# Kernel optimization log

Measured on AMD Instinct MI355X. Metric: run time of the kernel, lower is better.

## Reference

```python
import jax, jax.numpy as jnp
import numpy as np
from jax import lax

DIM = 64           # LHMSA dim
C3 = 3 * DIM       # high-band channels
HEADS = C3 // 32   # 6
WS = 8             # window size
SHIFT = 4          # shift size
EPS = 1e-6


def _ln_chw(x, w, b):
    # channel-last layer norm applied to BCHW input over C
    xt = x.transpose(0, 2, 3, 1)
    mu = xt.mean(-1, keepdims=True)
    var = ((xt - mu) ** 2).mean(-1, keepdims=True)
    y = (xt - mu) / jnp.sqrt(var + EPS) * w + b
    return y.transpose(0, 3, 1, 2)


def _conv1x1(x, w):
    # w: (out_c, in_c), no bias
    return jnp.einsum('bchw,oc->bohw', x, w)


def _dwconv3(x, w):
    # depthwise 3x3, w: (C,1,3,3)
    C = x.shape[1]
    return lax.conv_general_dilated(x, w, (1, 1), ((1, 1), (1, 1)),
                                    dimension_numbers=('NCHW', 'OIHW', 'NCHW'),
                                    feature_group_count=C)


def _gelu(x):
    return jax.nn.gelu(x, approximate=False)


def _dwt(x):
    x01 = x[:, :, 0::2, :] * 0.5
    x02 = x[:, :, 1::2, :] * 0.5
    x1 = x01[:, :, :, 0::2]; x2 = x02[:, :, :, 0::2]
    x3 = x01[:, :, :, 1::2]; x4 = x02[:, :, :, 1::2]
    ll = x1 + x2 + x3 + x4
    high = jnp.concatenate([-x1 - x2 + x3 + x4,
                            -x1 + x2 - x3 + x4,
                            x1 - x2 - x3 + x4], axis=1)
    return ll, high


def _iwt(ll, high):
    B, C, H, W = ll.shape
    hl, lh, hh = jnp.split(high, 3, axis=1)
    x1 = (ll - hl - lh + hh) * 0.5
    x2 = (ll - hl + lh - hh) * 0.5
    x3 = (ll + hl - lh - hh) * 0.5
    x4 = (ll + hl + lh + hh) * 0.5
    even = jnp.stack([x1, x3], axis=-1).reshape(B, C, H, 2 * W)  # rows 0::2
    odd = jnp.stack([x2, x4], axis=-1).reshape(B, C, H, 2 * W)   # rows 1::2
    return jnp.stack([even, odd], axis=-2).reshape(B, C, 2 * H, 2 * W)


def _swin_mhsa(x, qkv_w, qkv_b, proj_w, proj_b, rpb_table, rpi):
    # x: (B, C3, H, W); H,W divisible by WS -> no padding path
    B, C, H, W = x.shape
    dh = C // HEADS
    scale = dh ** (-0.5)
    xh = x.transpose(0, 2, 3, 1)                           # BHWC
    xh = jnp.roll(xh, (-SHIFT, -SHIFT), axis=(1, 2))
    nh, nw = H // WS, W // WS
    xw = xh.reshape(B, nh, WS, nw, WS, C).transpose(0, 1, 3, 2, 4, 5)
    xw = xw.reshape(B * nh * nw, WS * WS, C)               # (nW, N, C)
    qkv = xw @ qkv_w.T + qkv_b                             # (nW, N, 3C)
    qkv = qkv.reshape(-1, WS * WS, 3, HEADS, dh).transpose(2, 0, 3, 1, 4)
    q, k, v = qkv[0], qkv[1], qkv[2]                       # (nW, h, N, dh)
    attn = jnp.einsum('whnd,whmd->whnm', q, k) * scale
    bias = rpb_table[rpi.reshape(-1)].reshape(WS * WS, WS * WS, HEADS)
    attn = jax.nn.softmax(attn + bias.transpose(2, 0, 1)[None], axis=-1)
    out = jnp.einsum('whnm,whmd->whnd', attn, v)
    out = out.transpose(0, 2, 1, 3).reshape(-1, WS * WS, C)
    out = out.reshape(B, nh, nw, WS, WS, C).transpose(0, 1, 3, 2, 4, 5)
    out = out.reshape(B, H, W, C)
    out = jnp.roll(out, (SHIFT, SHIFT), axis=(1, 2))
    out = out @ proj_w.T + proj_b
    return out.transpose(0, 3, 1, 2)


def _rel_pos_index():
    coords = np.stack(np.meshgrid(np.arange(WS), np.arange(WS), indexing='ij'))
    cf = coords.reshape(2, -1)
    rel = (cf[:, :, None] - cf[:, None, :]).transpose(1, 2, 0).astype(np.int64)
    rel[:, :, 0] += WS - 1
    rel[:, :, 1] += WS - 1
    rel[:, :, 0] *= 2 * WS - 1
    return rel.sum(-1)


def setup_inputs() -> dict:
    key = jax.random.key(0)
    ks = jax.random.split(key, 12)
    B, H, W = 2, 512, 512
    x = jax.random.normal(ks[0], (B, DIM, H, W), jnp.float32)
    s = 0.02
    inp = {
        'x': x,
        'norm_w': jnp.ones((C3,), jnp.float32),
        'norm_b': jnp.zeros((C3,), jnp.float32),
        'qkv_w': jax.random.normal(ks[1], (3 * C3, C3), jnp.float32) * s,
        'qkv_b': jnp.zeros((3 * C3,), jnp.float32),
        'proj_w': jax.random.normal(ks[2], (C3, C3), jnp.float32) * s,
        'proj_b': jnp.zeros((C3,), jnp.float32),
        'rpb_table': jax.random.normal(ks[3], ((2 * WS - 1) ** 2, HEADS), jnp.float32) * s,
        'aux_dw_w': jax.random.normal(ks[4], (DIM, 1, 3, 3), jnp.float32) * 0.1,
        'aux_pw_w': jax.random.normal(ks[5], (DIM, DIM), jnp.float32) * s,
        'cg1_w': jax.random.normal(ks[6], (C3 * 3 // 12, DIM), jnp.float32) * s,
        'cg2_w': jax.random.normal(ks[7], (C3, C3 * 3 // 12), jnp.float32) * s,
        'po_w': jax.random.normal(ks[8], (DIM, DIM), jnp.float32) * s,
        'gamma_main': jnp.full((1,), 1e-4, jnp.float32),
        'gamma_aux': jnp.full((1,), 0.5, jnp.float32),
        'gamma_cross': jnp.full((1,), 1e-5, jnp.float32),
        'rel_pos_index': jnp.asarray(_rel_pos_index(), jnp.int32),
    }
    return inp


def reference(x, norm_w, norm_b, qkv_w, qkv_b, proj_w, proj_b, rpb_table,
              aux_dw_w, aux_pw_w, cg1_w, cg2_w, po_w,
              gamma_main, gamma_aux, gamma_cross, rel_pos_index):
    ll, high = _dwt(x)
    high_norm = _ln_chw(high, norm_w, norm_b)
    refined_high = high + gamma_main * _swin_mhsa(high_norm, qkv_w, qkv_b,
                                                  proj_w, proj_b, rpb_table,
                                                  rel_pos_index)
    refined_ll = ll + gamma_aux * _conv1x1(_gelu(_dwconv3(ll, aux_dw_w)), aux_pw_w)
    gap = ll.mean((2, 3), keepdims=True)
    cross = jax.nn.sigmoid(_conv1x1(_gelu(_conv1x1(gap, cg1_w)), cg2_w))
    refined_high = refined_high * (1.0 + gamma_cross * (cross - 0.5) * 2.0)
    out = _iwt(refined_ll, refined_high)
    return _conv1x1(out - x, po_w)
```

## Files before the change

### kernel.cpp

```cpp
#include <hip/hip_runtime.h>
#include <hip/hip_bf16.h>
#include <math.h>

typedef __hip_bfloat16 bf16;
typedef short s8v __attribute__((ext_vector_type(8)));
typedef float f4v __attribute__((ext_vector_type(4)));
#define MFMA16(a,b,c) __builtin_amdgcn_mfma_f32_16x16x32_bf16(a,b,c,0,0,0)

#define B2   2
#define C64  64
#define C3   192
#define HEADS 6
#define NWIN 2048

#define P_NORMW 0
#define P_NORMB 192
#define P_QKVW  384
#define P_QKVB  110976
#define P_PROJW 111552
#define P_PROJB 148416
#define P_RPB   148608
#define P_AUXDW 149958
#define P_AUXPW 150534
#define P_CG1   154630
#define P_CG2   157702
#define P_PO    166918
#define P_GM    171014
#define P_GA    171015
#define P_GC    171016

#define WS_FLAG   0
#define WS_PARAMS 256
#define WS_GAP    684544
#define WS_AMUL   685568
#define WS_CVAL   687616
#define WS_TSTAT  689664
#define WS_LL     1738240
#define WS_DLLW   18515456
#define WS_WOUT   35292672
#define WS_HRAW   85624320
#define WS_WQKV   135955968
#define WS_WPROJ  136177152
#define WS_WPW    136250880
#define WS_WPO    136259072
#define WS_S12    136267264
#define WS_BIAS6  136271872

__device__ __forceinline__ float bfu(unsigned short u){
  return __uint_as_float(((unsigned)u) << 16);
}
template<bool ISF>
__device__ __forceinline__ float4 LD4(const void* p, long i){
  if constexpr (ISF) return *(const float4*)((const float*)p + i);
  else {
    const ushort4 u = *(const ushort4*)((const bf16*)p + i);
    float4 r; r.x = bfu(u.x); r.y = bfu(u.y); r.z = bfu(u.z); r.w = bfu(u.w);
    return r;
  }
}
template<bool ISF>
__device__ __forceinline__ void ST(void* p, long i, float v){
  if constexpr (ISF) ((float*)p)[i] = v;
  else ((bf16*)p)[i] = __float2bfloat16(v);
}
__device__ __forceinline__ float gelu_f(float x){
  const float z = 0.7978845608028654f * (x + 0.044715f * x*x*x);
  const float t = 1.f - 2.f / (__expf(2.f*z) + 1.f);
  return 0.5f * x * (1.f + t);
}
__device__ __forceinline__ unsigned pk2(float a, float b){
  return (unsigned)__bfloat16_as_ushort(__float2bfloat16(a)) |
         ((unsigned)__bfloat16_as_ushort(__float2bfloat16(b)) << 16);
}
__device__ __forceinline__ uint4 pk8(const float* v){
  uint4 r;
  r.x = pk2(v[0], v[1]); r.y = pk2(v[2], v[3]);
  r.z = pk2(v[4], v[5]); r.w = pk2(v[6], v[7]);
  return r;
}
__device__ __forceinline__ void gld16(const void* g, void* l){
  __builtin_amdgcn_global_load_lds(
      (const __attribute__((address_space(1))) void*)g,
      (__attribute__((address_space(3))) void*)l, 16, 0, 0);
}

__global__ __launch_bounds__(256) void detect_kernel(const void* x, int* flag){
  __shared__ int wildcnt;
  if (threadIdx.x == 0) wildcnt = 0;
  __syncthreads();
  const unsigned short* u = (const unsigned short*)x;
  int wild = 0;
  for (int i = threadIdx.x; i < 2048; i += 256){
    unsigned int v = ((unsigned int)u[i]) << 16;
    float f = __uint_as_float(v);
    float a = fabsf(f);
    if (!(a < 1e8f) || (a > 0.f && a < 1e-8f)) wild++;
  }
  atomicAdd(&wildcnt, wild);
  __syncthreads();
  if (threadIdx.x == 0) *flag = (wildcnt > 100) ? 1 : 0;
}

struct PP { const void* src[15]; float* dst[15]; int n[15]; };
__global__ __launch_bounds__(256) void convert_params(PP pp, const int* flag){
  const bool isf = (*flag) != 0;
  const int gid = blockIdx.x*256 + threadIdx.x;
  const int gsz = gridDim.x*256;
#pragma unroll
  for (int q = 0; q < 15; q++){
    const int n = pp.n[q];
    const void* s = pp.src[q];
    float* d = pp.dst[q];
    for (int i = gid; i < n; i += gsz)
      d[i] = isf ? ((const float*)s)[i] : __bfloat162float(((const bf16*)s)[i]);
  }
}

__global__ __launch_bounds__(256) void kw_convert(const float* pf, const int* rpi,
                                                  bf16* wqkvF, bf16* wproj,
                                                  bf16* wpw, bf16* wpo, float* bias6T){
  const int i = blockIdx.x*256 + threadIdx.x;
  if (i < 110592){
    const int c = i % 192;
    wqkvF[i] = __float2bfloat16(pf[P_QKVW + i] * pf[P_NORMW + c]);
  } else if (i < 147456)  wproj[i-110592] = __float2bfloat16(pf[P_PROJW + (i-110592)]);
  else if (i < 151552)    wpw[i-147456]   = __float2bfloat16(pf[P_AUXPW + (i-147456)]);
  else if (i < 155648)    wpo[i-151552]   = __float2bfloat16(pf[P_PO + (i-151552)]);
  else if (i < 180224){
    const int j = i - 155648;
    const int hh = j >> 12, nm = j & 4095;
    const int row = nm >> 6, col = nm & 63;
    bias6T[hh*4096 + col*64 + row] = pf[P_RPB + rpi[nm]*6 + hh];
  }
}

__global__ __launch_bounds__(256) void k0d_s12(const float* pf, float2* s12p){
  const int o = blockIdx.x*16 + (threadIdx.x >> 4);
  const int lane = threadIdx.x & 15;
  if (o >= 576) return;
  float s1 = 0.f, s2 = 0.f;
  for (int c = lane; c < 192; c += 16){
    const float w = pf[P_QKVW + o*192 + c];
    s1 += w * pf[P_NORMW + c];
    s2 += w * pf[P_NORMB + c];
  }
  s1 += __shfl_xor(s1,1,16); s1 += __shfl_xor(s1,2,16);
  s1 += __shfl_xor(s1,4,16); s1 += __shfl_xor(s1,8,16);
  s2 += __shfl_xor(s2,1,16); s2 += __shfl_xor(s2,2,16);
  s2 += __shfl_xor(s2,4,16); s2 += __shfl_xor(s2,8,16);
  if (lane == 0){
    float2 v; v.x = s1; v.y = s2 + pf[P_QKVB + o];
    s12p[o] = v;
  }
}

template<bool ISF>
__device__ void k1f_body(const void* xv, bf16* llb, bf16* hraw, float2* tstat){
  const int wid = blockIdx.x;
  const int b  = wid >> 10;
  const int wh = (wid >> 5) & 31;
  const int ww = wid & 31;
  const int tid = threadIdx.x;
  const int tp = tid >> 3, l8 = tid & 7;
  const int t0 = tp*2;
  const int wi = t0 >> 3, wj0 = t0 & 7;
  const int h2 = (wh*8 + wi + 4) & 255;
  const int w2 = (ww*8 + wj0 + 4) & 255;
  const long rowbase = ((long)(2*h2) << 9) + 2*w2;
  float r0[3][8], r1[3][8];
  float s0 = 0.f, q0 = 0.f, s1 = 0.f, q1 = 0.f;
#pragma unroll
  for (int cc = 0; cc < 8; ++cc){
    const int c = l8*8 + cc;
    const long base = ((long)(b*64 + c) << 18) + rowbase;
    const float4 ta = LD4<ISF>(xv, base);
    const float4 tb = LD4<ISF>(xv, base + 512);
    float a = ta.x, cr = ta.y, bb = tb.x, dd = tb.y;
    const float ll0 = 0.5f*(a + bb + cr + dd);
    const float h00 = 0.5f*(-a - bb + cr + dd);
    const float h10 = 0.5f*(-a + bb - cr + dd);
    const float h20 = 0.5f*( a - bb - cr + dd);
    r0[0][cc] = h00; r0[1][cc] = h10; r0[2][cc] = h20;
    s0 += h00 + h10 + h20; q0 += h00*h00 + h10*h10 + h20*h20;
    a = ta.z; cr = ta.w; bb = tb.z; dd = tb.w;
    const float ll1 = 0.5f*(a + bb + cr + dd);
    const float h01 = 0.5f*(-a - bb + cr + dd);
    const float h11 = 0.5f*(-a + bb - cr + dd);
    const float h21 = 0.5f*( a - bb - cr + dd);
    r1[0][cc] = h01; r1[1][cc] = h11; r1[2][cc] = h21;
    s1 += h01 + h11 + h21; q1 += h01*h01 + h11*h11 + h21*h21;
    *(unsigned*)(llb + ((long)(b*64 + c) << 16) + ((long)h2 << 8) + w2) = pk2(ll0, ll1);
  }
  const long hb = ((long)wid*64 + t0)*192 + l8*8;
  *(uint4*)(hraw + hb)            = pk8(r0[0]);
  *(uint4*)(hraw + hb + 64)       = pk8(r0[1]);
  *(uint4*)(hraw + hb + 128)      = pk8(r0[2]);
  *(uint4*)(hraw + hb + 192)      = pk8(r1[0]);
  *(uint4*)(hraw + hb + 192 + 64) = pk8(r1[1]);
  *(uint4*)(hraw + hb + 192 +128) = pk8(r1[2]);
  s0 += __shfl_xor(s0,1,8); s0 += __shfl_xor(s0,2,8); s0 += __shfl_xor(s0,4,8);
  q0 += __shfl_xor(q0,1,8); q0 += __shfl_xor(q0,2,8); q0 += __shfl_xor(q0,4,8);
  s1 += __shfl_xor(s1,1,8); s1 += __shfl_xor(s1,2,8); s1 += __shfl_xor(s1,4,8);
  q1 += __shfl_xor(q1,1,8); q1 += __shfl_xor(q1,2,8); q1 += __shfl_xor(q1,4,8);
  if (l8 == 0){
    float mean = s0 * (1.f/192.f);
    float var = fmaxf(q0 * (1.f/192.f) - mean*mean, 0.f);
    float rstd = rsqrtf(var + 1e-6f);
    float2 st; st.x = rstd; st.y = mean * rstd;
    tstat[wid*64 + t0] = st;
    mean = s1 * (1.f/192.f);
    var = fmaxf(q1 * (1.f/192.f) - mean*mean, 0.f);
    rstd = rsqrtf(var + 1e-6f);
    st.x = rstd; st.y = mean * rstd;
    tstat[wid*64 + t0 + 1] = st;
  }
}
__global__ __launch_bounds__(256,4) void k1f_dwt(const void* xv, bf16* llb, bf16* hraw,
                                                 float2* tstat, const int* flag){
  if (*flag) k1f_body<true>(xv, llb, hraw, tstat);
  else       k1f_body<false>(xv, llb, hraw, tstat);
}

__global__ __launch_bounds__(256) void k3_cross(const float* pf, const float* gap,
                                                float* amul, float* cval){
  __shared__ float t1[B2][48];
  __shared__ float g[B2][64];
  const int tid = threadIdx.x;
  if (tid < 128) g[tid >> 6][tid & 63] = gap[tid];
  __syncthreads();
  if (tid < 96){
    const int b = tid / 48, j = tid % 48;
    float s = 0.f;
    const float* w = pf + P_CG1 + j * 64;
    for (int c = 0; c < 64; ++c) s += w[c] * g[b][c];
    t1[b][j] = gelu_f(s);
  }
  __syncthreads();
  const float gm = pf[P_GM], gc = pf[P_GC];
  for (int o = tid; o < B2 * C3; o += 256){
    const int b = o / C3, ch = o % C3;
    float s = 0.f;
    const float* w = pf + P_CG2 + ch * 48;
    for (int j = 0; j < 48; ++j) s += w[j] * t1[b][j];
    const float cr = 1.f / (1.f + expf(-s));
    const float c = gc * (cr - 0.5f) * 2.f;
    cval[o] = c;
    amul[o] = gm * (1.f + c);
  }
}


__device__ void k4_body(char* sm, int g, const bf16* hraw, const float2* tstat,
                        const bf16* wqkvF, const float2* s12p, const float* bias6T,
                        bf16* wout){
  bf16* bstage = (bf16*)sm;
  const int xcd = g & 7, slot = g >> 3;
  const int pair = (slot/6)*8 + xcd;
  const int h    = slot - (slot/6)*6;
  const int tid = threadIdx.x;
  const int wv5 = tid >> 6;
  const int lw  = wv5 >> 2;
  const int rg  = wv5 & 3;
  const int l = tid & 63, lr = l & 15, lg = l >> 4;
  const int wid = pair*2 + lw;
  char* reg = sm + 36864 + lw*13312;
  bf16* bq = (bf16*)reg;
  bf16* bk = (bf16*)(reg + 4608);
  char* vtb = reg + 9216;
  bf16* bp = (bf16*)reg;
  const f4v fz = {0.f,0.f,0.f,0.f};
  const float scale = 0.17677669529663687f;
  const bf16* at = hraw + (long)wid * 12288;

#pragma unroll
  for (int pass = 0; pass < 5; ++pass){
    if (pass*512 + wv5*64 < 2304){
      const int idx = pass*512 + tid;
      const int rl  = idx / 24;
      const int off = (idx - rl*24) * 16;
      const int soff = off ^ ((rl & 7) << 4);
      const int grow = (rl >> 5)*192 + h*32 + (rl & 31);
      gld16(wqkvF + grow*192 + (soff >> 1),
            (char*)bstage + (pass*512 + wv5*64)*16);
    }
  }
  s8v aA[6];
#pragma unroll
  for (int ks = 0; ks < 6; ++ks)
    aA[ks] = *(const s8v*)(at + (rg*16+lr)*192 + ks*32 + lg*8);
  float2 st4[4];
#pragma unroll
  for (int i = 0; i < 4; ++i)
    st4[i] = tstat[wid*64 + rg*16 + lg*4 + i];
  __syncthreads();

  f4v acc[6];
#pragma unroll
  for (int nt = 0; nt < 6; ++nt) acc[nt] = fz;
#pragma unroll
  for (int ks = 0; ks < 6; ++ks){
    const int kb = (ks*32 + lg*8) * 2;
#pragma unroll
    for (int nt = 0; nt < 6; ++nt){
      const int row = nt*16 + lr;
      const s8v bfr = *(const s8v*)((const char*)bstage + row*384 + (kb ^ ((row&7)<<4)));
      acc[nt] = MFMA16(aA[ks], bfr, acc[nt]);
    }
  }
#pragma unroll
  for (int nt = 0; nt < 6; ++nt){
    const int ol = nt*16 + lr;
    const int p = ol >> 5, c = ol & 31;
    const int ocol = p*192 + h*32 + c;
    const float2 sp = s12p[ocol];
#pragma unroll
    for (int i = 0; i < 4; ++i){
      const int row = rg*16 + lg*4 + i;
      const float v = st4[i].x*acc[nt][i] - st4[i].y*sp.x + sp.y;
      if (p == 0)      bq[row*36 + c] = __float2bfloat16(v*scale);
      else if (p == 1) bk[row*36 + c] = __float2bfloat16(v);
      else             *(bf16*)(vtb + ((c*128 + row*2) ^ ((c&7)<<4))) = __float2bfloat16(v);
    }
  }
  __syncthreads();

  f4v sacc[4];
  {
    const s8v a = *(const s8v*)(bq + (rg*16+lr)*36 + lg*8);
#pragma unroll
    for (int nt = 0; nt < 4; ++nt){
      const s8v bfr = *(const s8v*)(bk + (nt*16+lr)*36 + lg*8);
      sacc[nt] = MFMA16(a, bfr, fz);
    }
  }
  f4v bld[4];
#pragma unroll
  for (int nt = 0; nt < 4; ++nt)
    bld[nt] = *(const f4v*)(bias6T + h*4096 + (nt*16+lr)*64 + rg*16 + lg*4);
  float pvv[4][4];
  float inv4[4];
#pragma unroll
  for (int i = 0; i < 4; ++i){
    float s = 0.f;
#pragma unroll
    for (int nt = 0; nt < 4; ++nt){
      const float e = __expf(sacc[nt][i] + bld[nt][i]);
      pvv[i][nt] = e;
      s += e;
    }
    s += __shfl_xor(s, 1, 16);
    s += __shfl_xor(s, 2, 16);
    s += __shfl_xor(s, 4, 16);
    s += __shfl_xor(s, 8, 16);
    inv4[i] = 1.f/s;
  }
  __syncthreads();

#pragma unroll
  for (int i = 0; i < 4; ++i){
    const int row = rg*16 + lg*4 + i;
#pragma unroll
    for (int nt = 0; nt < 4; ++nt)
      bp[row*72 + nt*16 + lr] = __float2bfloat16(pvv[i][nt]);
  }
  f4v oacc[2] = {fz, fz};
#pragma unroll
  for (int ks2 = 0; ks2 < 2; ++ks2){
    const s8v a = *(const s8v*)(bp + (rg*16+lr)*72 + ks2*32 + lg*8);
#pragma unroll
    for (int nn = 0; nn < 2; ++nn){
      const int d = nn*16 + lr;
      const s8v bfr = *(const s8v*)(vtb + ((d*128 + (ks2*32+lg*8)*2) ^ ((d&7)<<4)));
      oacc[nn] = MFMA16(a, bfr, oacc[nn]);
    }
  }
#pragma unroll
  for (int nn = 0; nn < 2; ++nn)
#pragma unroll
    for (int i = 0; i < 4; ++i){
      const int row = rg*16 + lg*4 + i;
      wout[((long)wid*64 + row)*192 + h*32 + nn*16 + lr] =
        __float2bfloat16(oacc[nn][i] * inv4[i]);
    }
}

__device__ void k6f_body(char* smb, int blk6, const bf16* llb, const float* pf,
                         const bf16* wpw, bf16* dllw){
  const int tid = threadIdx.x;
  const int sub = tid >> 8;
  const int t2 = tid & 255;
  char* sm6 = smb + sub*24576;
  bf16* tile = (bf16*)sm6;
  bf16* t    = (bf16*)(sm6 + 15360);
  const int tl = blk6*2 + sub;
  const int b = tl >> 10, ti = (tl >> 5) & 31, tj = tl & 31;
  const int y0 = ti*8 - 1;
  const int x0 = tj*8 - 2;

  for (int e = t2; e < 7680; e += 256){
    const int col = e % 12;
    const int rc  = e / 12;
    const int row = rc % 10, ch = rc / 10;
    const int x = x0 + col, y = y0 + row;
    bf16 v = __float2bfloat16(0.f);
    if ((unsigned)x < 256u && (unsigned)y < 256u)
      v = llb[((long)(b*64 + ch) << 16) + ((long)y << 8) + x];
    tile[rc*12 + col] = v;
  }
  __syncthreads();

  {
    const int tok = t2 & 63, cgrp = t2 >> 6;
    const int iy = tok >> 3, ix = tok & 7;
#pragma unroll
    for (int cc = 0; cc < 16; ++cc){
      const int c = cgrp*16 + cc;
      const float* wk = pf + P_AUXDW + c*9;
      float s = 0.f;
#pragma unroll
      for (int ky = 0; ky < 3; ++ky)
#pragma unroll
        for (int kx = 0; kx < 3; ++kx)
          s += wk[ky*3 + kx] * __bfloat162float(tile[(c*10 + iy + ky)*12 + ix + 1 + kx]);
      t[tok*72 + c] = __float2bfloat16(gelu_f(s));
    }
  }
  __syncthreads();

  const int wv = t2 >> 6, l = t2 & 63, lr = l & 15, lg = l >> 4;
  const f4v fz = {0.f,0.f,0.f,0.f};
  f4v acc[4];
#pragma unroll
  for (int nt = 0; nt < 4; ++nt) acc[nt] = fz;
#pragma unroll
  for (int ks = 0; ks < 2; ++ks){
    const s8v a = *(const s8v*)(t + (wv*16+lr)*72 + ks*32 + lg*8);
#pragma unroll
    for (int nt = 0; nt < 4; ++nt){
      const s8v bfr = *(const s8v*)(wpw + (nt*16+lr)*64 + ks*32 + lg*8);
      acc[nt] = MFMA16(a, bfr, acc[nt]);
    }
  }
  const float ga = pf[P_GA];
#pragma unroll
  for (int i = 0; i < 4; ++i){
    const int p = wv*16 + lg*4 + i;
    const int y = ti*8 + (p >> 3), x = tj*8 + (p & 7);
    const int sy = (y - 4) & 255, sx = (x - 4) & 255;
    const int wd = b*1024 + (sy >> 3)*32 + (sx >> 3);
    const int tok2 = (sy & 7)*8 + (sx & 7);
    const long ob = ((long)wd*64 + tok2)*64;
#pragma unroll
    for (int nt = 0; nt < 4; ++nt)
      dllw[ob + nt*16 + lr] = __float2bfloat16(ga * acc[nt][i]);
  }
}

__device__ void k2_body(char* smb, int bc, const bf16* llb, float* gap){
  float* red = (float*)smb;
  const int tid = threadIdx.x;
  const uint4* p = (const uint4*)(llb + ((long)bc << 16));
  float s = 0.f;
  for (int i = tid; i < 8192; i += 512){
    const uint4 v = p[i];
    s += __uint_as_float(v.x << 16) + __uint_as_float(v.x & 0xffff0000u);
    s += __uint_as_float(v.y << 16) + __uint_as_float(v.y & 0xffff0000u);
    s += __uint_as_float(v.z << 16) + __uint_as_float(v.z & 0xffff0000u);
    s += __uint_as_float(v.w << 16) + __uint_as_float(v.w & 0xffff0000u);
  }
  red[tid] = s; __syncthreads();
  for (int st = 256; st > 0; st >>= 1){
    if (tid < st) red[tid] += red[tid + st];
    __syncthreads();
  }
  if (tid == 0) gap[bc] = red[0] * (1.f / 65536.f);
}

__global__ __launch_bounds__(512,4) void kmix(const bf16* hraw, const float2* tstat,
                                              const bf16* wqkvF, const float2* s12p,
                                              const float* bias6T, bf16* wout,
                                              const bf16* llb, const float* pf,
                                              const bf16* wpw, bf16* dllw, float* gap){
  __shared__ __align__(16) char sm[63488];
  const int blk = blockIdx.x;
  if (blk < 7168){
    const int g7 = blk / 7, r7 = blk - g7*7;
    if (r7 < 6) k4_body(sm, g7*6 + r7, hraw, tstat, wqkvF, s12p, bias6T, wout);
    else        k6f_body(sm, g7, llb, pf, wpw, dllw);
  } else {
    k2_body(sm, blk - 7168, llb, gap);
  }
}

__global__ __launch_bounds__(256,5) void k5_proj(bf16* wout, const bf16* hraw,
                                                 const bf16* wproj, const float* pf,
                                                 const float* amul, const float* cval){
  __shared__ __align__(16) bf16 bufC[64*192];
  const int wid = blockIdx.x;
  const int b  = wid >> 10;
  const int tid = threadIdx.x;
  const int wv = tid >> 6, l = tid & 63, lr = l & 15, lg = l >> 4;

  {
    const bf16* hsrc = hraw + (long)wid * 12288;
#pragma unroll
    for (int pass = 0; pass < 6; ++pass){
      const int idx = pass*256 + tid;
      const int row = idx / 24;
      const int off = (idx % 24) * 16;
      const int soff = off ^ ((row & 7) << 4);
      gld16(hsrc + row*192 + (soff >> 1),
            (char*)bufC + (pass*256 + wv*64)*16);
    }
  }

  const f4v fz = {0.f,0.f,0.f,0.f};
  const bf16* at = wout + (long)wid * 12288;

  f4v acc[3][4];
#pragma unroll
  for (int nt = 0; nt < 3; ++nt)
#pragma unroll
    for (int mt = 0; mt < 4; ++mt) acc[nt][mt] = fz;
#pragma unroll
  for (int ks = 0; ks < 6; ++ks){
    const int k0 = ks*32;
    s8v a[4];
#pragma unroll
    for (int mt = 0; mt < 4; ++mt)
      a[mt] = *(const s8v*)(at + (mt*16+lr)*192 + k0 + lg*8);
#pragma unroll
    for (int nt = 0; nt < 3; ++nt){
      const int ocol = (wv*3+nt)*16 + lr;
      const s8v bfr = *(const s8v*)(wproj + ocol*192 + k0 + lg*8);
#pragma unroll
      for (int mt = 0; mt < 4; ++mt) acc[nt][mt] = MFMA16(a[mt], bfr, acc[nt][mt]);
    }
  }
  __syncthreads();
#pragma unroll
  for (int nt = 0; nt < 3; ++nt){
    const int col = (wv*3+nt)*16 + lr;
    const int bc = b*192 + col;
    const float am = amul[bc], cv = cval[bc], pb = pf[P_PROJB + col];
#pragma unroll
    for (int mt = 0; mt < 4; ++mt)
#pragma unroll
      for (int i = 0; i < 4; ++i){
        const int row = mt*16 + lg*4 + i;
        const float hv = __bfloat162float(
          *(const bf16*)((const char*)bufC + row*384 + ((col*2) ^ ((row&7)<<4))));
        wout[(long)wid*12288 + row*192 + col] =
          __float2bfloat16(am*(acc[nt][mt][i] + pb) + cv*hv);
      }
  }
}

template<bool ISF>
__device__ void k7_body(const bf16* dvalw, const bf16* dllw, const bf16* wpo,
                        void* out, char* yp){
  const int blk = blockIdx.x;
  const int b = blk >> 10, hh = (blk >> 1) & 511, half = blk & 1;
  const int h2 = hh >> 1, posH = hh & 1;
  const int th = (h2 + 252) & 255;
  const int wh = th >> 3, wi = th & 7;
  const int tid = threadIdx.x;
  const int j = tid & 7;
#pragma unroll
  for (int pass = 0; pass < 8; ++pass){
    const int p = pass*32 + (tid >> 3);
    const int ww2 = half*256 + p;
    const int w2 = ww2 >> 1, posW = ww2 & 1;
    const int tw = (w2 + 252) & 255;
    const int ww = tw >> 3, wj = tw & 7;
    const int wid = b*1024 + wh*32 + ww;
    const int tok = wi*8 + wj;
    const long dvb = ((long)wid*64 + tok)*192 + j*8;
    const s8v hl8 = *(const s8v*)(dvalw + dvb);
    const s8v lh8 = *(const s8v*)(dvalw + dvb + 64);
    const s8v hh8 = *(const s8v*)(dvalw + dvb + 128);
    const s8v dl8 = *(const s8v*)(dllw + ((long)wid*64 + tok)*64 + j*8);
    const float s1 = posW ? 0.5f : -0.5f;
    const float s2 = posH ? 0.5f : -0.5f;
    const float s3 = posW == posH ? 0.5f : -0.5f;
    float e[8];
#pragma unroll
    for (int q = 0; q < 8; ++q)
      e[q] = 0.5f*bfu((unsigned short)dl8[q]) + s1*bfu((unsigned short)hl8[q])
           + s2*bfu((unsigned short)lh8[q]) + s3*bfu((unsigned short)hh8[q]);
    *(uint4*)(yp + ((p*128 + j*16) ^ ((p&7)<<4))) = pk8(e);
  }
  __syncthreads();
  const int wv = tid >> 6, l = tid & 63, lr = l & 15, lg = l >> 4;
  const f4v fz = {0.f,0.f,0.f,0.f};
  f4v acc[4][4];
#pragma unroll
  for (int mt = 0; mt < 4; ++mt)
#pragma unroll
    for (int nt = 0; nt < 4; ++nt) acc[mt][nt] = fz;
#pragma unroll
  for (int ks = 0; ks < 2; ++ks){
    const int k0 = ks*32;
    s8v a[4];
#pragma unroll
    for (int mt = 0; mt < 4; ++mt)
      a[mt] = *(const s8v*)(wpo + (mt*16+lr)*64 + k0 + lg*8);
#pragma unroll
    for (int nt = 0; nt < 4; ++nt){
      const int prow = wv*64 + nt*16 + lr;
      const s8v bfr = *(const s8v*)(yp + ((prow*128 + (k0+lg*8)*2) ^ ((prow&7)<<4)));
#pragma unroll
      for (int mt = 0; mt < 4; ++mt) acc[mt][nt] = MFMA16(a[mt], bfr, acc[mt][nt]);
    }
  }
  const int px0 = half*256 + wv*64;
#pragma unroll
  for (int mt = 0; mt < 4; ++mt)
#pragma unroll
    for (int nt = 0; nt < 4; ++nt)
#pragma unroll
      for (int i = 0; i < 4; ++i){
        const int c = mt*16 + lg*4 + i;
        const long ob = ((long)(b*64 + c)*512 + hh)*512 + px0 + nt*16 + lr;
        ST<ISF>(out, ob, acc[mt][nt][i]);
      }
}
__global__ __launch_bounds__(256,4) void k7_out(const bf16* dvalw, const bf16* dllw,
                                                const bf16* wpo, void* out, const int* flag){
  __shared__ __align__(16) char yp[32768];
  if (*flag) k7_body<true>(dvalw, dllw, wpo, out, yp);
  else       k7_body<false>(dvalw, dllw, wpo, out, yp);
}

extern "C" void kernel_launch(void* const* d_in, const int* in_sizes, int n_in,
                              void* d_out, int out_size, void* d_ws, size_t ws_size,
                              hipStream_t stream){
  char* ws = (char*)d_ws;
  int*   flag = (int*)(ws + WS_FLAG);
  float* pf   = (float*)(ws + WS_PARAMS);
  float* gap  = (float*)(ws + WS_GAP);
  float* amul = (float*)(ws + WS_AMUL);
  float* cval = (float*)(ws + WS_CVAL);
  float2* tstat=(float2*)(ws + WS_TSTAT);
  bf16*  llb  = (bf16*)(ws + WS_LL);
  bf16*  dllw = (bf16*)(ws + WS_DLLW);
  bf16*  wout = (bf16*)(ws + WS_WOUT);
  bf16*  hraw = (bf16*)(ws + WS_HRAW);
  bf16*  wqkvF= (bf16*)(ws + WS_WQKV);
  bf16*  wproj= (bf16*)(ws + WS_WPROJ);
  bf16*  wpw  = (bf16*)(ws + WS_WPW);
  bf16*  wpo  = (bf16*)(ws + WS_WPO);
  float2* s12p= (float2*)(ws + WS_S12);
  float* bias6= (float*)(ws + WS_BIAS6);
  const int* rpi = (const int*)d_in[16];

  detect_kernel<<<1, 256, 0, stream>>>(d_in[0], flag);

  PP pp;
  const int pidx[15] = {1,2,3,4,5,6,7,8,9,10,11,12,13,14,15};
  const int poff[15] = {P_NORMW,P_NORMB,P_QKVW,P_QKVB,P_PROJW,P_PROJB,P_RPB,
                        P_AUXDW,P_AUXPW,P_CG1,P_CG2,P_PO,P_GM,P_GA,P_GC};
  for (int q = 0; q < 15; q++){
    pp.src[q] = d_in[pidx[q]];
    pp.dst[q] = pf + poff[q];
    pp.n[q]   = in_sizes[pidx[q]];
  }
  convert_params<<<128, 256, 0, stream>>>(pp, flag);
  kw_convert<<<704, 256, 0, stream>>>(pf, rpi, wqkvF, wproj, wpw, wpo, bias6);
  k0d_s12  <<<36,  256, 0, stream>>>(pf, s12p);

  k1f_dwt<<<NWIN, 256, 0, stream>>>(d_in[0], llb, hraw, tstat, flag);
  kmix   <<<7296, 512, 0, stream>>>(hraw, tstat, wqkvF, s12p, bias6, wout,
                                    llb, pf, wpw, dllw, gap);
  k3_cross<<<1,   256, 0, stream>>>(pf, gap, amul, cval);
  k5_proj<<<NWIN, 256, 0, stream>>>(wout, hraw, wproj, pf, amul, cval);
  k7_out <<<2048, 256, 0, stream>>>(wout, dllw, wpo, d_out, flag);
}
```

Measured before the change: 395.2 us.

## Fuse projection into output kernel and merge parameter prep kernels

The windowed projection GEMM (k5) moves into the final IWT+1x1 output kernel, so the refined high-band values are combined with the low band in registers and written straight to shared memory. This removes a full write and re-read of the window-output buffer. The three parameter-prep kernels are merged into one, reading the raw inputs directly, and the relative-position bias is fed as the MFMA accumulator init instead of a separate add. In exchange, occupancy drops to 2 blocks per CU because of the larger shared-memory footprint. Each block also reloads the wproj tiles and hraw rows from global memory.

```diff
diff --git a/kernel.cpp b/kernel.cpp
--- a/kernel.cpp
+++ b/kernel.cpp
@@ -49,6 +49,9 @@
 __device__ __forceinline__ float bfu(unsigned short u){
   return __uint_as_float(((unsigned)u) << 16);
 }
+__device__ __forceinline__ float LDR(const void* p, long i, bool isf){
+  return isf ? ((const float*)p)[i] : bfu(((const unsigned short*)p)[i]);
+}
 template<bool ISF>
 __device__ __forceinline__ float4 LD4(const void* p, long i){
   if constexpr (ISF) return *(const float4*)((const float*)p + i);
@@ -102,7 +105,9 @@
 }
 
 struct PP { const void* src[15]; float* dst[15]; int n[15]; };
-__global__ __launch_bounds__(256) void convert_params(PP pp, const int* flag){
+__global__ __launch_bounds__(256) void kprep(PP pp, const int* flag, const int* rpi,
+                                             bf16* wqkvF, bf16* wproj, bf16* wpw,
+                                             bf16* wpo, float* bias6T, float2* s12p){
   const bool isf = (*flag) != 0;
   const int gid = blockIdx.x*256 + threadIdx.x;
   const int gsz = gridDim.x*256;
@@ -111,46 +116,32 @@
     const int n = pp.n[q];
     const void* s = pp.src[q];
     float* d = pp.dst[q];
-    for (int i = gid; i < n; i += gsz)
-      d[i] = isf ? ((const float*)s)[i] : __bfloat162float(((const bf16*)s)[i]);
-  }
-}
-
-__global__ __launch_bounds__(256) void kw_convert(const float* pf, const int* rpi,
-                                                  bf16* wqkvF, bf16* wproj,
-                                                  bf16* wpw, bf16* wpo, float* bias6T){
-  const int i = blockIdx.x*256 + threadIdx.x;
-  if (i < 110592){
-    const int c = i % 192;
-    wqkvF[i] = __float2bfloat16(pf[P_QKVW + i] * pf[P_NORMW + c]);
-  } else if (i < 147456)  wproj[i-110592] = __float2bfloat16(pf[P_PROJW + (i-110592)]);
-  else if (i < 151552)    wpw[i-147456]   = __float2bfloat16(pf[P_AUXPW + (i-147456)]);
-  else if (i < 155648)    wpo[i-151552]   = __float2bfloat16(pf[P_PO + (i-151552)]);
-  else if (i < 180224){
-    const int j = i - 155648;
+    for (int i = gid; i < n; i += gsz) d[i] = LDR(s, i, isf);
+  }
+  const void* qkvw = pp.src[2];
+  const void* normw = pp.src[0];
+  for (int i = gid; i < 110592; i += gsz)
+    wqkvF[i] = __float2bfloat16(LDR(qkvw, i, isf) * LDR(normw, i % 192, isf));
+  for (int i = gid; i < 36864; i += gsz)
+    wproj[i] = __float2bfloat16(LDR(pp.src[4], i, isf));
+  for (int i = gid; i < 4096; i += gsz){
+    wpw[i] = __float2bfloat16(LDR(pp.src[8], i, isf));
+    wpo[i] = __float2bfloat16(LDR(pp.src[11], i, isf));
+  }
+  for (int j = gid; j < 24576; j += gsz){
     const int hh = j >> 12, nm = j & 4095;
     const int row = nm >> 6, col = nm & 63;
-    bias6T[hh*4096 + col*64 + row] = pf[P_RPB + rpi[nm]*6 + hh];
-  }
-}
-
-__global__ __launch_bounds__(256) void k0d_s12(const float* pf, float2* s12p){
-  const int o = blockIdx.x*16 + (threadIdx.x >> 4);
-  const int lane = threadIdx.x & 15;
-  if (o >= 576) return;
-  float s1 = 0.f, s2 = 0.f;
-  for (int c = lane; c < 192; c += 16){
-    const float w = pf[P_QKVW + o*192 + c];
-    s1 += w * pf[P_NORMW + c];
-    s2 += w * pf[P_NORMB + c];
-  }
-  s1 += __shfl_xor(s1,1,16); s1 += __shfl_xor(s1,2,16);
-  s1 += __shfl_xor(s1,4,16); s1 += __shfl_xor(s1,8,16);
-  s2 += __shfl_xor(s2,1,16); s2 += __shfl_xor(s2,2,16);
-  s2 += __shfl_xor(s2,4,16); s2 += __shfl_xor(s2,8,16);
-  if (lane == 0){
-    float2 v; v.x = s1; v.y = s2 + pf[P_QKVB + o];
-    s12p[o] = v;
+    bias6T[hh*4096 + col*64 + row] = LDR(pp.src[6], rpi[nm]*6 + hh, isf);
+  }
+  if (gid < 576){
+    float s1 = 0.f, s2 = 0.f;
+    for (int c = 0; c < 192; ++c){
+      const float w = LDR(qkvw, gid*192 + c, isf);
+      s1 += w * LDR(normw, c, isf);
+      s2 += w * LDR(pp.src[1], c, isf);
+    }
+    float2 v; v.x = s1; v.y = s2 + LDR(pp.src[3], gid, isf);
+    s12p[gid] = v;
   }
 }
 
@@ -249,7 +240,6 @@
   }
 }
 
-
 __device__ void k4_body(char* sm, int g, const bf16* hraw, const float2* tstat,
                         const bf16* wqkvF, const float2* s12p, const float* bias6T,
                         bf16* wout){
@@ -324,19 +314,19 @@
   }
   __syncthreads();
 
+  f4v bld[4];
+#pragma unroll
+  for (int nt = 0; nt < 4; ++nt)
+    bld[nt] = *(const f4v*)(bias6T + h*4096 + (nt*16+lr)*64 + rg*16 + lg*4);
   f4v sacc[4];
   {
     const s8v a = *(const s8v*)(bq + (rg*16+lr)*36 + lg*8);
 #pragma unroll
     for (int nt = 0; nt < 4; ++nt){
       const s8v bfr = *(const s8v*)(bk + (nt*16+lr)*36 + lg*8);
-      sacc[nt] = MFMA16(a, bfr, fz);
-    }
-  }
-  f4v bld[4];
-#pragma unroll
-  for (int nt = 0; nt < 4; ++nt)
-    bld[nt] = *(const f4v*)(bias6T + h*4096 + (nt*16+lr)*64 + rg*16 + lg*4);
+      sacc[nt] = MFMA16(a, bfr, bld[nt]);
+    }
+  }
   float pvv[4][4];
   float inv4[4];
 #pragma unroll
@@ -344,7 +334,7 @@
     float s = 0.f;
 #pragma unroll
     for (int nt = 0; nt < 4; ++nt){
-      const float e = __expf(sacc[nt][i] + bld[nt][i]);
+      const float e = __expf(sacc[nt][i]);
       pvv[i][nt] = e;
       s += e;
     }
@@ -492,112 +482,100 @@
   }
 }
 
-__global__ __launch_bounds__(256,5) void k5_proj(bf16* wout, const bf16* hraw,
-                                                 const bf16* wproj, const float* pf,
-                                                 const float* amul, const float* cval){
-  __shared__ __align__(16) bf16 bufC[64*192];
-  const int wid = blockIdx.x;
-  const int b  = wid >> 10;
-  const int tid = threadIdx.x;
-  const int wv = tid >> 6, l = tid & 63, lr = l & 15, lg = l >> 4;
-
-  {
-    const bf16* hsrc = hraw + (long)wid * 12288;
-#pragma unroll
-    for (int pass = 0; pass < 6; ++pass){
-      const int idx = pass*256 + tid;
-      const int row = idx / 24;
-      const int off = (idx % 24) * 16;
-      const int soff = off ^ ((row & 7) << 4);
-      gld16(hsrc + row*192 + (soff >> 1),
-            (char*)bufC + (pass*256 + wv*64)*16);
-    }
-  }
-
-  const f4v fz = {0.f,0.f,0.f,0.f};
-  const bf16* at = wout + (long)wid * 12288;
-
-  f4v acc[3][4];
-#pragma unroll
-  for (int nt = 0; nt < 3; ++nt)
-#pragma unroll
-    for (int mt = 0; mt < 4; ++mt) acc[nt][mt] = fz;
-#pragma unroll
-  for (int ks = 0; ks < 6; ++ks){
-    const int k0 = ks*32;
-    s8v a[4];
-#pragma unroll
-    for (int mt = 0; mt < 4; ++mt)
-      a[mt] = *(const s8v*)(at + (mt*16+lr)*192 + k0 + lg*8);
-#pragma unroll
-    for (int nt = 0; nt < 3; ++nt){
-      const int ocol = (wv*3+nt)*16 + lr;
-      const s8v bfr = *(const s8v*)(wproj + ocol*192 + k0 + lg*8);
-#pragma unroll
-      for (int mt = 0; mt < 4; ++mt) acc[nt][mt] = MFMA16(a[mt], bfr, acc[nt][mt]);
-    }
-  }
-  __syncthreads();
-#pragma unroll
-  for (int nt = 0; nt < 3; ++nt){
-    const int col = (wv*3+nt)*16 + lr;
-    const int bc = b*192 + col;
-    const float am = amul[bc], cv = cval[bc], pb = pf[P_PROJB + col];
-#pragma unroll
-    for (int mt = 0; mt < 4; ++mt)
-#pragma unroll
-      for (int i = 0; i < 4; ++i){
-        const int row = mt*16 + lg*4 + i;
-        const float hv = __bfloat162float(
-          *(const bf16*)((const char*)bufC + row*384 + ((col*2) ^ ((row&7)<<4))));
-        wout[(long)wid*12288 + row*192 + col] =
-          __float2bfloat16(am*(acc[nt][mt][i] + pb) + cv*hv);
-      }
-  }
-}
-
 template<bool ISF>
-__device__ void k7_body(const bf16* dvalw, const bf16* dllw, const bf16* wpo,
-                        void* out, char* yp){
+__device__ void k57_body(const bf16* wout, const bf16* hraw, const bf16* dllw,
+                         const bf16* wproj, const bf16* wpo, const float* pf,
+                         const float* amul, const float* cval, void* out, char* sm){
+  char* ypb = sm;
+  bf16* hst = (bf16*)(sm + 32768);
   const int blk = blockIdx.x;
   const int b = blk >> 10, hh = (blk >> 1) & 511, half = blk & 1;
   const int h2 = hh >> 1, posH = hh & 1;
   const int th = (h2 + 252) & 255;
   const int wh = th >> 3, wi = th & 7;
   const int tid = threadIdx.x;
-  const int j = tid & 7;
-#pragma unroll
-  for (int pass = 0; pass < 8; ++pass){
-    const int p = pass*32 + (tid >> 3);
-    const int ww2 = half*256 + p;
-    const int w2 = ww2 >> 1, posW = ww2 & 1;
-    const int tw = (w2 + 252) & 255;
-    const int ww = tw >> 3, wj = tw & 7;
-    const int wid = b*1024 + wh*32 + ww;
-    const int tok = wi*8 + wj;
-    const long dvb = ((long)wid*64 + tok)*192 + j*8;
-    const s8v hl8 = *(const s8v*)(dvalw + dvb);
-    const s8v lh8 = *(const s8v*)(dvalw + dvb + 64);
-    const s8v hh8 = *(const s8v*)(dvalw + dvb + 128);
-    const s8v dl8 = *(const s8v*)(dllw + ((long)wid*64 + tok)*64 + j*8);
-    const float s1 = posW ? 0.5f : -0.5f;
-    const float s2 = posH ? 0.5f : -0.5f;
-    const float s3 = posW == posH ? 0.5f : -0.5f;
-    float e[8];
-#pragma unroll
-    for (int q = 0; q < 8; ++q)
-      e[q] = 0.5f*bfu((unsigned short)dl8[q]) + s1*bfu((unsigned short)hl8[q])
-           + s2*bfu((unsigned short)lh8[q]) + s3*bfu((unsigned short)hh8[q]);
-    *(uint4*)(yp + ((p*128 + j*16) ^ ((p&7)<<4))) = pk8(e);
-  }
-  __syncthreads();
   const int wv = tid >> 6, l = tid & 63, lr = l & 15, lg = l >> 4;
   const f4v fz = {0.f,0.f,0.f,0.f};
-  f4v acc[4][4];
+  const float sH = posH ? 0.5f : -0.5f;
+  const long wrow0 = (long)(b*1024 + wh*32);
+
+  float amv[12], cvv[12], pbv[12];
+#pragma unroll
+  for (int nt = 0; nt < 12; ++nt){
+    const int col = nt*16 + lr;
+    amv[nt] = amul[b*192 + col];
+    cvv[nt] = cval[b*192 + col];
+    pbv[nt] = pf[P_PROJB + col];
+  }
+
+#pragma unroll
+  for (int ck = 0; ck < 2; ++ck){
+    const int w2base = half*128 + ck*64;
+#pragma unroll
+    for (int pass = 0; pass < 6; ++pass){
+      const int idx = pass*256 + tid;
+      const int r   = idx / 24;
+      const int off = (idx - r*24) * 16;
+      const int soff = off ^ ((r & 7) << 4);
+      const int tw = (w2base + r + 252) & 255;
+      const long src = (wrow0 + (tw >> 3))*12288 + (wi*8 + (tw & 7))*192;
+      gld16(hraw + src + (soff >> 1), (char*)hst + (pass*256 + wv*64)*16);
+    }
+    const int rA = wv*16 + lr;
+    const int twA = (w2base + rA + 252) & 255;
+    const bf16* arow = wout + (wrow0 + (twA >> 3))*12288 + (wi*8 + (twA & 7))*192;
+    s8v aA[6];
+#pragma unroll
+    for (int ks = 0; ks < 6; ++ks)
+      aA[ks] = *(const s8v*)(arow + ks*32 + lg*8);
+    __syncthreads();
+
+    f4v acc[12];
+#pragma unroll
+    for (int nt = 0; nt < 12; ++nt) acc[nt] = fz;
+#pragma unroll
+    for (int ks = 0; ks < 6; ++ks){
+      const int k0 = ks*32;
+#pragma unroll
+      for (int nt = 0; nt < 12; ++nt){
+        const s8v bfr = *(const s8v*)(wproj + (nt*16+lr)*192 + k0 + lg*8);
+        acc[nt] = MFMA16(aA[ks], bfr, acc[nt]);
+      }
+    }
+#pragma unroll
+    for (int i = 0; i < 4; ++i){
+      const int rowo = wv*16 + lg*4 + i;
+      const int tw2 = (w2base + rowo + 252) & 255;
+      const long dlb = ((wrow0 + (tw2 >> 3))*64 + wi*8 + (tw2 & 7))*64;
+      const int p0 = ck*128 + 2*rowo;
+      const int sw0 = (p0 & 7) << 4, sw1 = ((p0+1) & 7) << 4;
+#pragma unroll
+      for (int nt2 = 0; nt2 < 4; ++nt2){
+        const int c = nt2*16 + lr;
+        const int hb = rowo*384;
+        const int rsw = (rowo & 7) << 4;
+        const float hv0 = bfu(*(const unsigned short*)((const char*)hst + hb + ((c*2) ^ rsw)));
+        const float hv1 = bfu(*(const unsigned short*)((const char*)hst + hb + (((64+c)*2) ^ rsw)));
+        const float hv2 = bfu(*(const unsigned short*)((const char*)hst + hb + (((128+c)*2) ^ rsw)));
+        const float dvc  = amv[nt2]  *(acc[nt2][i]  + pbv[nt2])   + cvv[nt2]  *hv0;
+        const float dv64 = amv[nt2+4]*(acc[nt2+4][i]+ pbv[nt2+4]) + cvv[nt2+4]*hv1;
+        const float dv128= amv[nt2+8]*(acc[nt2+8][i]+ pbv[nt2+8]) + cvv[nt2+8]*hv2;
+        const float dl = __bfloat162float(dllw[dlb + c]);
+        const float common = 0.5f*dl + sH*dv64;
+        const float e0 = common - 0.5f*dvc - sH*dv128;
+        const float e1 = common + 0.5f*dvc + sH*dv128;
+        *(bf16*)(ypb + ((p0*128     + c*2) ^ sw0)) = __float2bfloat16(e0);
+        *(bf16*)(ypb + (((p0+1)*128 + c*2) ^ sw1)) = __float2bfloat16(e1);
+      }
+    }
+    __syncthreads();
+  }
+
+  f4v acc2[4][4];
 #pragma unroll
   for (int mt = 0; mt < 4; ++mt)
 #pragma unroll
-    for (int nt = 0; nt < 4; ++nt) acc[mt][nt] = fz;
+    for (int nt = 0; nt < 4; ++nt) acc2[mt][nt] = fz;
 #pragma unroll
   for (int ks = 0; ks < 2; ++ks){
     const int k0 = ks*32;
@@ -608,9 +586,9 @@
 #pragma unroll
     for (int nt = 0; nt < 4; ++nt){
       const int prow = wv*64 + nt*16 + lr;
-      const s8v bfr = *(const s8v*)(yp + ((prow*128 + (k0+lg*8)*2) ^ ((prow&7)<<4)));
-#pragma unroll
-      for (int mt = 0; mt < 4; ++mt) acc[mt][nt] = MFMA16(a[mt], bfr, acc[mt][nt]);
+      const s8v bfr = *(const s8v*)(ypb + ((prow*128 + (k0+lg*8)*2) ^ ((prow&7)<<4)));
+#pragma unroll
+      for (int mt = 0; mt < 4; ++mt) acc2[mt][nt] = MFMA16(a[mt], bfr, acc2[mt][nt]);
     }
   }
   const int px0 = half*256 + wv*64;
@@ -622,14 +600,17 @@
       for (int i = 0; i < 4; ++i){
         const int c = mt*16 + lg*4 + i;
         const long ob = ((long)(b*64 + c)*512 + hh)*512 + px0 + nt*16 + lr;
-        ST<ISF>(out, ob, acc[mt][nt][i]);
+        ST<ISF>(out, ob, acc2[mt][nt][i]);
       }
 }
-__global__ __launch_bounds__(256,4) void k7_out(const bf16* dvalw, const bf16* dllw,
-                                                const bf16* wpo, void* out, const int* flag){
-  __shared__ __align__(16) char yp[32768];
-  if (*flag) k7_body<true>(dvalw, dllw, wpo, out, yp);
-  else       k7_body<false>(dvalw, dllw, wpo, out, yp);
+__global__ __launch_bounds__(256,2) void k57_out(const bf16* wout, const bf16* hraw,
+                                                 const bf16* dllw, const bf16* wproj,
+                                                 const bf16* wpo, const float* pf,
+                                                 const float* amul, const float* cval,
+                                                 void* out, const int* flag){
+  __shared__ __align__(16) char sm[57344];
+  if (*flag) k57_body<true>(wout, hraw, dllw, wproj, wpo, pf, amul, cval, out, sm);
+  else       k57_body<false>(wout, hraw, dllw, wproj, wpo, pf, amul, cval, out, sm);
 }
 
 extern "C" void kernel_launch(void* const* d_in, const int* in_sizes, int n_in,
@@ -665,14 +646,12 @@
     pp.dst[q] = pf + poff[q];
     pp.n[q]   = in_sizes[pidx[q]];
   }
-  convert_params<<<128, 256, 0, stream>>>(pp, flag);
-  kw_convert<<<704, 256, 0, stream>>>(pf, rpi, wqkvF, wproj, wpw, wpo, bias6);
-  k0d_s12  <<<36,  256, 0, stream>>>(pf, s12p);
+  kprep<<<512, 256, 0, stream>>>(pp, flag, rpi, wqkvF, wproj, wpw, wpo, bias6, s12p);
 
   k1f_dwt<<<NWIN, 256, 0, stream>>>(d_in[0], llb, hraw, tstat, flag);
   kmix   <<<7296, 512, 0, stream>>>(hraw, tstat, wqkvF, s12p, bias6, wout,
                                     llb, pf, wpw, dllw, gap);
   k3_cross<<<1,   256, 0, stream>>>(pf, gap, amul, cval);
-  k5_proj<<<NWIN, 256, 0, stream>>>(wout, hraw, wproj, pf, amul, cval);
-  k7_out <<<2048, 256, 0, stream>>>(wout, dllw, wpo, d_out, flag);
-}
+  k57_out<<<2048, 256, 0, stream>>>(wout, hraw, dllw, wproj, wpo, pf,
+                                    amul, cval, d_out, flag);
+}
```

Result: slower. 528.6 us (+33.8%).

## Fuse parameter prep kernels into DWT launch and fold bias into MFMA accumulator

Applied to the files above, without the earlier changes.

Merges three parameter-conversion kernels (convert_params, kw_convert, k0d_s12) into extra blocks of the DWT kernel, so prep reads raw inputs directly and runs alongside the DWT instead of in three serialized launches. It also loads the relative position bias before the QK MFMA and uses it as the accumulator initial value, which removes an add per score element. The cost is 512 extra blocks inside the DWT grid that do strided loops. The s12 computation now re-reads raw weights with per-element format branching.

```diff
diff --git a/kernel.cpp b/kernel.cpp
--- a/kernel.cpp
+++ b/kernel.cpp
@@ -49,6 +49,9 @@
 __device__ __forceinline__ float bfu(unsigned short u){
   return __uint_as_float(((unsigned)u) << 16);
 }
+__device__ __forceinline__ float LDR(const void* p, long i, bool isf){
+  return isf ? ((const float*)p)[i] : bfu(((const unsigned short*)p)[i]);
+}
 template<bool ISF>
 __device__ __forceinline__ float4 LD4(const void* p, long i){
   if constexpr (ISF) return *(const float4*)((const float*)p + i);
@@ -102,61 +105,54 @@
 }
 
 struct PP { const void* src[15]; float* dst[15]; int n[15]; };
-__global__ __launch_bounds__(256) void convert_params(PP pp, const int* flag){
-  const bool isf = (*flag) != 0;
-  const int gid = blockIdx.x*256 + threadIdx.x;
-  const int gsz = gridDim.x*256;
+__device__ void kprep_body(int vblk, const PP& pp, bool isf, const int* rpi,
+                           bf16* wqkvF, bf16* wproj, bf16* wpw,
+                           bf16* wpo, float* bias6T, float2* s12p){
+  const int gid = vblk*256 + threadIdx.x;
+  const int gsz = 512*256;
 #pragma unroll
   for (int q = 0; q < 15; q++){
     const int n = pp.n[q];
     const void* s = pp.src[q];
     float* d = pp.dst[q];
-    for (int i = gid; i < n; i += gsz)
-      d[i] = isf ? ((const float*)s)[i] : __bfloat162float(((const bf16*)s)[i]);
-  }
-}
-
-__global__ __launch_bounds__(256) void kw_convert(const float* pf, const int* rpi,
-                                                  bf16* wqkvF, bf16* wproj,
-                                                  bf16* wpw, bf16* wpo, float* bias6T){
-  const int i = blockIdx.x*256 + threadIdx.x;
-  if (i < 110592){
-    const int c = i % 192;
-    wqkvF[i] = __float2bfloat16(pf[P_QKVW + i] * pf[P_NORMW + c]);
-  } else if (i < 147456)  wproj[i-110592] = __float2bfloat16(pf[P_PROJW + (i-110592)]);
-  else if (i < 151552)    wpw[i-147456]   = __float2bfloat16(pf[P_AUXPW + (i-147456)]);
-  else if (i < 155648)    wpo[i-151552]   = __float2bfloat16(pf[P_PO + (i-151552)]);
-  else if (i < 180224){
-    const int j = i - 155648;
+    for (int i = gid; i < n; i += gsz) d[i] = LDR(s, i, isf);
+  }
+  const void* qkvw = pp.src[2];
+  const void* normw = pp.src[0];
+  for (int i = gid; i < 110592; i += gsz)
+    wqkvF[i] = __float2bfloat16(LDR(qkvw, i, isf) * LDR(normw, i % 192, isf));
+  for (int i = gid; i < 36864; i += gsz)
+    wproj[i] = __float2bfloat16(LDR(pp.src[4], i, isf));
+  for (int i = gid; i < 4096; i += gsz){
+    wpw[i] = __float2bfloat16(LDR(pp.src[8], i, isf));
+    wpo[i] = __float2bfloat16(LDR(pp.src[11], i, isf));
+  }
+  for (int j = gid; j < 24576; j += gsz){
     const int hh = j >> 12, nm = j & 4095;
     const int row = nm >> 6, col = nm & 63;
-    bias6T[hh*4096 + col*64 + row] = pf[P_RPB + rpi[nm]*6 + hh];
-  }
-}
-
-__global__ __launch_bounds__(256) void k0d_s12(const float* pf, float2* s12p){
-  const int o = blockIdx.x*16 + (threadIdx.x >> 4);
-  const int lane = threadIdx.x & 15;
-  if (o >= 576) return;
-  float s1 = 0.f, s2 = 0.f;
-  for (int c = lane; c < 192; c += 16){
-    const float w = pf[P_QKVW + o*192 + c];
-    s1 += w * pf[P_NORMW + c];
-    s2 += w * pf[P_NORMB + c];
-  }
-  s1 += __shfl_xor(s1,1,16); s1 += __shfl_xor(s1,2,16);
-  s1 += __shfl_xor(s1,4,16); s1 += __shfl_xor(s1,8,16);
-  s2 += __shfl_xor(s2,1,16); s2 += __shfl_xor(s2,2,16);
-  s2 += __shfl_xor(s2,4,16); s2 += __shfl_xor(s2,8,16);
-  if (lane == 0){
-    float2 v; v.x = s1; v.y = s2 + pf[P_QKVB + o];
-    s12p[o] = v;
+    bias6T[hh*4096 + col*64 + row] = LDR(pp.src[6], rpi[nm]*6 + hh, isf);
+  }
+  const int o = gid >> 4, lane = gid & 15;
+  if (o < 576){
+    float s1 = 0.f, s2 = 0.f;
+    for (int c = lane; c < 192; c += 16){
+      const float w = LDR(qkvw, o*192 + c, isf);
+      s1 += w * LDR(normw, c, isf);
+      s2 += w * LDR(pp.src[1], c, isf);
+    }
+    s1 += __shfl_xor(s1,1,16); s1 += __shfl_xor(s1,2,16);
+    s1 += __shfl_xor(s1,4,16); s1 += __shfl_xor(s1,8,16);
+    s2 += __shfl_xor(s2,1,16); s2 += __shfl_xor(s2,2,16);
+    s2 += __shfl_xor(s2,4,16); s2 += __shfl_xor(s2,8,16);
+    if (lane == 0){
+      float2 v; v.x = s1; v.y = s2 + LDR(pp.src[3], o, isf);
+      s12p[o] = v;
+    }
   }
 }
 
 template<bool ISF>
-__device__ void k1f_body(const void* xv, bf16* llb, bf16* hraw, float2* tstat){
-  const int wid = blockIdx.x;
+__device__ void k1f_body(int wid, const void* xv, bf16* llb, bf16* hraw, float2* tstat){
   const int b  = wid >> 10;
   const int wh = (wid >> 5) & 31;
   const int ww = wid & 31;
@@ -215,10 +211,20 @@
     tstat[wid*64 + t0 + 1] = st;
   }
 }
-__global__ __launch_bounds__(256,4) void k1f_dwt(const void* xv, bf16* llb, bf16* hraw,
-                                                 float2* tstat, const int* flag){
-  if (*flag) k1f_body<true>(xv, llb, hraw, tstat);
-  else       k1f_body<false>(xv, llb, hraw, tstat);
+
+__global__ __launch_bounds__(256,4) void k1p(const void* xv, bf16* llb, bf16* hraw,
+                                             float2* tstat, const int* flag, PP pp,
+                                             const int* rpi, bf16* wqkvF, bf16* wproj,
+                                             bf16* wpw, bf16* wpo, float* bias6T,
+                                             float2* s12p){
+  const bool isf = (*flag) != 0;
+  const int blk = blockIdx.x;
+  if (blk < NWIN){
+    if (isf) k1f_body<true>(blk, xv, llb, hraw, tstat);
+    else     k1f_body<false>(blk, xv, llb, hraw, tstat);
+  } else {
+    kprep_body(blk - NWIN, pp, isf, rpi, wqkvF, wproj, wpw, wpo, bias6T, s12p);
+  }
 }
 
 __global__ __launch_bounds__(256) void k3_cross(const float* pf, const float* gap,
@@ -248,7 +254,6 @@
     amul[o] = gm * (1.f + c);
   }
 }
-
 
 __device__ void k4_body(char* sm, int g, const bf16* hraw, const float2* tstat,
                         const bf16* wqkvF, const float2* s12p, const float* bias6T,
@@ -324,19 +329,19 @@
   }
   __syncthreads();
 
+  f4v bld[4];
+#pragma unroll
+  for (int nt = 0; nt < 4; ++nt)
+    bld[nt] = *(const f4v*)(bias6T + h*4096 + (nt*16+lr)*64 + rg*16 + lg*4);
   f4v sacc[4];
   {
     const s8v a = *(const s8v*)(bq + (rg*16+lr)*36 + lg*8);
 #pragma unroll
     for (int nt = 0; nt < 4; ++nt){
       const s8v bfr = *(const s8v*)(bk + (nt*16+lr)*36 + lg*8);
-      sacc[nt] = MFMA16(a, bfr, fz);
-    }
-  }
-  f4v bld[4];
-#pragma unroll
-  for (int nt = 0; nt < 4; ++nt)
-    bld[nt] = *(const f4v*)(bias6T + h*4096 + (nt*16+lr)*64 + rg*16 + lg*4);
+      sacc[nt] = MFMA16(a, bfr, bld[nt]);
+    }
+  }
   float pvv[4][4];
   float inv4[4];
 #pragma unroll
@@ -344,7 +349,7 @@
     float s = 0.f;
 #pragma unroll
     for (int nt = 0; nt < 4; ++nt){
-      const float e = __expf(sacc[nt][i] + bld[nt][i]);
+      const float e = __expf(sacc[nt][i]);
       pvv[i][nt] = e;
       s += e;
     }
@@ -665,11 +670,9 @@
     pp.dst[q] = pf + poff[q];
     pp.n[q]   = in_sizes[pidx[q]];
   }
-  convert_params<<<128, 256, 0, stream>>>(pp, flag);
-  kw_convert<<<704, 256, 0, stream>>>(pf, rpi, wqkvF, wproj, wpw, wpo, bias6);
-  k0d_s12  <<<36,  256, 0, stream>>>(pf, s12p);
-
-  k1f_dwt<<<NWIN, 256, 0, stream>>>(d_in[0], llb, hraw, tstat, flag);
+
+  k1p    <<<NWIN + 512, 256, 0, stream>>>(d_in[0], llb, hraw, tstat, flag, pp, rpi,
+                                          wqkvF, wproj, wpw, wpo, bias6, s12p);
   kmix   <<<7296, 512, 0, stream>>>(hraw, tstat, wqkvF, s12p, bias6, wout,
                                     llb, pf, wpw, dllw, gap);
   k3_cross<<<1,   256, 0, stream>>>(pf, gap, amul, cval);
```

Result: faster. 379.0 us (-4.1%).
